# Optimization experiments

Hardware: AMD Instinct MI355X
Metric: run time of the kernel (lower is better)

## Reference

```python
import jax, jax.numpy as jnp
import numpy as np

B, T, NU, NX, NY = 16, 4096, 64, 256, 32

def setup_inputs() -> dict:
    key = jax.random.key(0)
    ks = jax.random.split(key, 7)
    s = 1.0 / np.sqrt(NX)
    return {
        "inputs": jax.random.normal(ks[0], (B, T, NU), dtype=jnp.float32),
        "h0": jax.random.uniform(ks[1], (B, NX), dtype=jnp.float32),
        "H_w": jax.random.normal(ks[2], (NX, NX), dtype=jnp.float32) * s,
        "H_b": jax.random.normal(ks[3], (NX,), dtype=jnp.float32) * s,
        "K_w": jax.random.normal(ks[4], (NX, NU), dtype=jnp.float32) * (1.0 / np.sqrt(NU)),
        "E_inv": jnp.eye(NX, dtype=jnp.float32),  # E = I in the original module
        "out_w": jax.random.normal(ks[5], (NY, NX), dtype=jnp.float32) * s,
        "out_b": jax.random.normal(ks[6], (NY,), dtype=jnp.float32) * s,
    }

def reference(inputs, h0, H_w, H_b, K_w, E_inv, out_w, out_b):
    # Precompute input projections for all steps: [B, T, NX]
    Ku = jnp.einsum("btu,xu->btx", inputs, K_w)
    seq_len = inputs.shape[1]

    def step(ht, ku_t):
        xt = ht @ H_w.T + H_b + ku_t          # Linear(H) + Linear(K)
        ht_new = jax.nn.relu(xt) @ E_inv      # nonlinearity then fixed matrix
        return ht_new, ht_new

    # loop runs seq_len - 1 times; states start with h0
    _, hs = jax.lax.scan(step, h0, jnp.swapaxes(Ku[:, : seq_len - 1, :], 0, 1))
    states = jnp.concatenate([h0[:, None, :], jnp.swapaxes(hs, 0, 1)], axis=1)  # [B, T, NX]
    yest = states @ out_w.T + out_b  # [B, T, NY]
    return (yest, states)
```

## Files before the change

kernel.cpp:

```cpp
#include <hip/hip_runtime.h>

#define Bsz 16
#define Tl  4096
#define NUc 64
#define NXc 256
#define NYc 32

template <int CTRL>
__device__ __forceinline__ float dpp_add(float x) {
    int y = __builtin_amdgcn_update_dpp(0, __float_as_int(x), CTRL, 0xf, 0xf, true);
    return x + __int_as_float(y);
}
__device__ __forceinline__ float reduce8(float x) {
    x = dpp_add<0xB1>(x);
    x = dpp_add<0x4E>(x);
    x = dpp_add<0x141>(x);
    return x;
}
__device__ __forceinline__ float row_reduce16(float x) {
    x = dpp_add<0x128>(x);
    x = dpp_add<0x124>(x);
    x = dpp_add<0x4E>(x);
    x = dpp_add<0xB1>(x);
    return x;
}

__device__ __forceinline__ void fast_barrier() {
    asm volatile("s_waitcnt lgkmcnt(0)\n\ts_barrier" ::: "memory");
}

#define KEEPF(x) asm volatile("" : "+v"(x))

#define DECLW(T,P) \
    float W##T##P##_0,W##T##P##_1,W##T##P##_2,W##T##P##_3,W##T##P##_4,W##T##P##_5,W##T##P##_6,W##T##P##_7, \
          W##T##P##_8,W##T##P##_9,W##T##P##_10,W##T##P##_11,W##T##P##_12,W##T##P##_13,W##T##P##_14,W##T##P##_15
#define LOADW(T,P,RP) { \
    const float* wr_ = (RP) + 16*P; \
    float4 a_=*(const float4*)(wr_+0), b_=*(const float4*)(wr_+4); \
    float4 c_=*(const float4*)(wr_+8), d_=*(const float4*)(wr_+12); \
    W##T##P##_0 =a_.x; W##T##P##_1 =a_.y; W##T##P##_2 =a_.z; W##T##P##_3 =a_.w; \
    W##T##P##_4 =b_.x; W##T##P##_5 =b_.y; W##T##P##_6 =b_.z; W##T##P##_7 =b_.w; \
    W##T##P##_8 =c_.x; W##T##P##_9 =c_.y; W##T##P##_10=c_.z; W##T##P##_11=c_.w; \
    W##T##P##_12=d_.x; W##T##P##_13=d_.y; W##T##P##_14=d_.z; W##T##P##_15=d_.w; }
#define PINW(T,P) \
    KEEPF(W##T##P##_0);  KEEPF(W##T##P##_1);  KEEPF(W##T##P##_2);  KEEPF(W##T##P##_3);  \
    KEEPF(W##T##P##_4);  KEEPF(W##T##P##_5);  KEEPF(W##T##P##_6);  KEEPF(W##T##P##_7);  \
    KEEPF(W##T##P##_8);  KEEPF(W##T##P##_9);  KEEPF(W##T##P##_10); KEEPF(W##T##P##_11); \
    KEEPF(W##T##P##_12); KEEPF(W##T##P##_13); KEEPF(W##T##P##_14); KEEPF(W##T##P##_15)

#define FMAQn(T,P,IA,IB,IC,ID,Q) \
    a##T##0 = fmaf(W##T##P##_##IA, (Q).x, a##T##0); \
    a##T##1 = fmaf(W##T##P##_##IB, (Q).y, a##T##1); \
    a##T##0 = fmaf(W##T##P##_##IC, (Q).z, a##T##0); \
    a##T##1 = fmaf(W##T##P##_##ID, (Q).w, a##T##1)
#define ROWFMA(T) \
    FMAQn(T,0, 0, 1, 2, 3, Q0); FMAQn(T,0, 4, 5, 6, 7, Q1); \
    FMAQn(T,0, 8, 9,10,11, Q2); FMAQn(T,0,12,13,14,15, Q3); \
    FMAQn(T,1, 0, 1, 2, 3, Q4); FMAQn(T,1, 4, 5, 6, 7, Q5); \
    FMAQn(T,1, 8, 9,10,11, Q6); FMAQn(T,1,12,13,14,15, Q7)

#define DECLK8(T) float kk##T##_0,kk##T##_1,kk##T##_2,kk##T##_3,kk##T##_4,kk##T##_5,kk##T##_6,kk##T##_7
#define LOADK8(T,RP) { \
    float4 a_=*(const float4*)(RP), b_=*(const float4*)((RP)+4); \
    kk##T##_0=a_.x; kk##T##_1=a_.y; kk##T##_2=a_.z; kk##T##_3=a_.w; \
    kk##T##_4=b_.x; kk##T##_5=b_.y; kk##T##_6=b_.z; kk##T##_7=b_.w; }
#define PINK8(T) \
    KEEPF(kk##T##_0); KEEPF(kk##T##_1); KEEPF(kk##T##_2); KEEPF(kk##T##_3); \
    KEEPF(kk##T##_4); KEEPF(kk##T##_5); KEEPF(kk##T##_6); KEEPF(kk##T##_7)
#define FMAK8(T) \
    a##T##0=fmaf(kk##T##_0,uu0.x,a##T##0); a##T##1=fmaf(kk##T##_1,uu0.y,a##T##1); \
    a##T##0=fmaf(kk##T##_2,uu0.z,a##T##0); a##T##1=fmaf(kk##T##_3,uu0.w,a##T##1); \
    a##T##0=fmaf(kk##T##_4,uu1.x,a##T##0); a##T##1=fmaf(kk##T##_5,uu1.y,a##T##1); \
    a##T##0=fmaf(kk##T##_6,uu1.z,a##T##0); a##T##1=fmaf(kk##T##_7,uu1.w,a##T##1)

#define KDECL4(Q)  float k##Q##_0, k##Q##_1, k##Q##_2, k##Q##_3
#define KLOAD4(Q) { float4 v_ = *(const float4*)(wr_ + 4*Q); \
    k##Q##_0 = v_.x; k##Q##_1 = v_.y; k##Q##_2 = v_.z; k##Q##_3 = v_.w; }
#define KPIN4(Q)   KEEPF(k##Q##_0); KEEPF(k##Q##_1); KEEPF(k##Q##_2); KEEPF(k##Q##_3)
#define KACC4(Q, U) { \
    s0_ = fmaf(k##Q##_0, (U).x, s0_); s1_ = fmaf(k##Q##_1, (U).y, s1_); \
    s0_ = fmaf(k##Q##_2, (U).z, s0_); s1_ = fmaf(k##Q##_3, (U).w, s1_); }

__global__ __launch_bounds__(256) void ku_kernel(const float* __restrict__ inputs,
                                                 const float* __restrict__ Kw,
                                                 float* __restrict__ Ku) {
    const int x    = threadIdx.x;
    const int row0 = blockIdx.x * 64;

    const float* wr_ = Kw + (size_t)x * NUc;
    KDECL4(0);  KDECL4(1);  KDECL4(2);  KDECL4(3);
    KDECL4(4);  KDECL4(5);  KDECL4(6);  KDECL4(7);
    KDECL4(8);  KDECL4(9);  KDECL4(10); KDECL4(11);
    KDECL4(12); KDECL4(13); KDECL4(14); KDECL4(15);
    KLOAD4(0);  KLOAD4(1);  KLOAD4(2);  KLOAD4(3);
    KLOAD4(4);  KLOAD4(5);  KLOAD4(6);  KLOAD4(7);
    KLOAD4(8);  KLOAD4(9);  KLOAD4(10); KLOAD4(11);
    KLOAD4(12); KLOAD4(13); KLOAD4(14); KLOAD4(15);
    KPIN4(0);  KPIN4(1);  KPIN4(2);  KPIN4(3);
    KPIN4(4);  KPIN4(5);  KPIN4(6);  KPIN4(7);
    KPIN4(8);  KPIN4(9);  KPIN4(10); KPIN4(11);
    KPIN4(12); KPIN4(13); KPIN4(14); KPIN4(15);

    __shared__ float sin_[64 * NUc];
    {
        const float* src = inputs + (size_t)row0 * NUc;
        #pragma unroll
        for (int i = 0; i < 16; ++i)
            sin_[threadIdx.x + i * 256] = src[threadIdx.x + i * 256];
    }
    __syncthreads();

    for (int r = 0; r < 64; ++r) {
        const float4* hp = (const float4*)(&sin_[r * NUc]);
        float s0_ = 0.f, s1_ = 0.f;
        KACC4(0,  hp[0]);  KACC4(1,  hp[1]);  KACC4(2,  hp[2]);  KACC4(3,  hp[3]);
        KACC4(4,  hp[4]);  KACC4(5,  hp[5]);  KACC4(6,  hp[6]);  KACC4(7,  hp[7]);
        KACC4(8,  hp[8]);  KACC4(9,  hp[9]);  KACC4(10, hp[10]); KACC4(11, hp[11]);
        KACC4(12, hp[12]); KACC4(13, hp[13]); KACC4(14, hp[14]); KACC4(15, hp[15]);
        Ku[(size_t)(row0 + r) * NXc + x] = s0_ + s1_;
    }
}

template <bool USE_KU>
__global__ __attribute__((amdgpu_flat_work_group_size(512, 512),
                          amdgpu_waves_per_eu(2, 2)))
void scan6(const float* __restrict__ Ku,
           const float* __restrict__ inputs,
           const float* __restrict__ Kw,
           const float* __restrict__ h0,
           const float* __restrict__ Hw,
           const float* __restrict__ Hb,
           float* __restrict__ states) {
    const int b   = blockIdx.x;
    const int tid = threadIdx.x;
    const int c   = tid & 7;
    const int jg  = tid >> 3;
    const int r0  = 4 * jg;
    const int row_w = r0 + (c & 3);

    __shared__ __align__(16) char shmem[4096];
    char* shm = shmem;
    float* shf = (float*)shmem;

    DECLW(A,0); DECLW(A,1); DECLW(B,0); DECLW(B,1);
    DECLW(C,0); DECLW(C,1); DECLW(D,0); DECLW(D,1);
    {
        const float* p = Hw + (size_t)r0 * NXc + 32 * c;
        LOADW(A,0,p); LOADW(A,1,p);  p += NXc;
        LOADW(B,0,p); LOADW(B,1,p);  p += NXc;
        LOADW(C,0,p); LOADW(C,1,p);  p += NXc;
        LOADW(D,0,p); LOADW(D,1,p);
    }
    DECLK8(A); DECLK8(B); DECLK8(C); DECLK8(D);
    const float* uptr = inputs + (size_t)b * Tl * NUc + 8 * c;
    if (!USE_KU) {
        const float* q = Kw + (size_t)r0 * NUc + 8 * c;
        LOADK8(A,q); q += NUc; LOADK8(B,q); q += NUc;
        LOADK8(C,q); q += NUc; LOADK8(D,q);
    }

    const float bias = Hb[row_w];

    const int wbyte  = 4 * (row_w + 4 * (row_w >> 5));
    const int rbase  = 144 * c;

    const float* kup = Ku + (size_t)b * Tl * NXc + NXc + row_w;
    float*       stp = states + (size_t)b * Tl * NXc + NXc + row_w;

    float bk;
    {
        float h = h0[b * NXc + row_w];
        states[(size_t)b * Tl * NXc + row_w] = h;
        shf[wbyte >> 2] = h;
        bk = USE_KU ? (bias + Ku[(size_t)b * Tl * NXc + row_w]) : bias;
        __syncthreads();
    }

#define STEPBODY(RD, WR) { \
    PINW(A,0); PINW(A,1); PINW(B,0); PINW(B,1); \
    PINW(C,0); PINW(C,1); PINW(D,0); PINW(D,1); \
    if (!USE_KU) { PINK8(A); PINK8(B); PINK8(C); PINK8(D); } \
    const char* rb = shm + (rbase + (RD)); \
    float4 Q0 = *(const float4*)(rb +   0); \
    float4 Q1 = *(const float4*)(rb +  16); \
    float4 Q2 = *(const float4*)(rb +  32); \
    float4 Q3 = *(const float4*)(rb +  48); \
    float4 Q4 = *(const float4*)(rb +  64); \
    float4 Q5 = *(const float4*)(rb +  80); \
    float4 Q6 = *(const float4*)(rb +  96); \
    float4 Q7 = *(const float4*)(rb + 112); \
    float kn_ = 0.f; float4 uu0, uu1; \
    if (USE_KU) { kn_ = *kup; kup += NXc; } \
    else { uu0 = *(const float4*)uptr; uu1 = *(const float4*)(uptr + 4); uptr += NUc; } \
    float aA0=0.f,aA1=0.f,aB0=0.f,aB1=0.f,aC0=0.f,aC1=0.f,aD0=0.f,aD1=0.f; \
    if (!USE_KU) { FMAK8(A); FMAK8(B); FMAK8(C); FMAK8(D); } \
    ROWFMA(A); ROWFMA(B); \
    float rA = reduce8(aA0 + aA1); \
    float rB = reduce8(aB0 + aB1); \
    ROWFMA(C); ROWFMA(D); \
    float rC = reduce8(aC0 + aC1); \
    float rD = reduce8(aD0 + aD1); \
    float x_ = (c & 1) ? rB : rA; \
    float y_ = (c & 1) ? rD : rC; \
    float v_ = (c & 2) ? y_ : x_; \
    float s_ = v_ + bk; \
    float h_ = s_ > 0.f ? s_ : 0.f; \
    *stp = h_; stp += NXc; \
    *(float*)(shm + (wbyte + (WR))) = h_; \
    bk = USE_KU ? (bias + kn_) : bias; \
    fast_barrier(); \
}

    for (int tt = 0; tt < (Tl - 2) / 2; ++tt) {
        STEPBODY(0, 2048);
        STEPBODY(2048, 0);
    }
    STEPBODY(0, 2048);
#undef STEPBODY
}

__global__ __launch_bounds__(512, 2) void yest2(const float* __restrict__ states,
                                                const float* __restrict__ ow,
                                                const float* __restrict__ obv,
                                                float* __restrict__ yest) {
    const int tid = threadIdx.x;
    const int c   = tid & 15;
    const int g   = tid >> 4;

    float y0_,y1_,y2_,y3_,y4_,y5_,y6_,y7_,y8_,y9_,y10_,y11_,y12_,y13_,y14_,y15_;
    {
        const float* wr = ow + (size_t)g * NXc + 16 * c;
        float4 vA = *(const float4*)(wr + 0),  vB = *(const float4*)(wr + 4);
        float4 vC = *(const float4*)(wr + 8),  vD = *(const float4*)(wr + 12);
        y0_=vA.x; y1_=vA.y; y2_ =vA.z; y3_ =vA.w;
        y4_=vB.x; y5_=vB.y; y6_ =vB.z; y7_ =vB.w;
        y8_=vC.x; y9_=vC.y; y10_=vC.z; y11_=vC.w;
        y12_=vD.x;y13_=vD.y;y14_=vD.z; y15_=vD.w;
        KEEPF(y0_); KEEPF(y1_); KEEPF(y2_);  KEEPF(y3_);
        KEEPF(y4_); KEEPF(y5_); KEEPF(y6_);  KEEPF(y7_);
        KEEPF(y8_); KEEPF(y9_); KEEPF(y10_); KEEPF(y11_);
        KEEPF(y12_);KEEPF(y13_);KEEPF(y14_); KEEPF(y15_);
    }
    const float ob = obv[g];

    const int row0 = blockIdx.x * 128;
    for (int r = 0; r < 128; r += 2) {
        const float* s0p = states + (size_t)(row0 + r) * NXc + 16 * c;
        const float* s1p = s0p + NXc;
        float4 A0 = *(const float4*)(s0p + 0), A1 = *(const float4*)(s0p + 4);
        float4 A2 = *(const float4*)(s0p + 8), A3 = *(const float4*)(s0p + 12);
        float4 B0 = *(const float4*)(s1p + 0), B1 = *(const float4*)(s1p + 4);
        float4 B2 = *(const float4*)(s1p + 8), B3 = *(const float4*)(s1p + 12);
        float acc0 = y0_*A0.x + y1_*A0.y + y2_*A0.z + y3_*A0.w
                   + y4_*A1.x + y5_*A1.y + y6_*A1.z + y7_*A1.w
                   + y8_*A2.x + y9_*A2.y + y10_*A2.z + y11_*A2.w
                   + y12_*A3.x + y13_*A3.y + y14_*A3.z + y15_*A3.w;
        float acc1 = y0_*B0.x + y1_*B0.y + y2_*B0.z + y3_*B0.w
                   + y4_*B1.x + y5_*B1.y + y6_*B1.z + y7_*B1.w
                   + y8_*B2.x + y9_*B2.y + y10_*B2.z + y11_*B2.w
                   + y12_*B3.x + y13_*B3.y + y14_*B3.z + y15_*B3.w;
        acc0 = row_reduce16(acc0);
        acc1 = row_reduce16(acc1);
        if (c == 0) {
            yest[(size_t)(row0 + r)     * NYc + g] = acc0 + ob;
            yest[(size_t)(row0 + r + 1) * NYc + g] = acc1 + ob;
        }
    }
}

extern "C" void kernel_launch(void* const* d_in, const int* in_sizes, int n_in,
                              void* d_out, int out_size, void* d_ws, size_t ws_size,
                              hipStream_t stream) {
    const float* inputs = (const float*)d_in[0];
    const float* h0     = (const float*)d_in[1];
    const float* Hw     = (const float*)d_in[2];
    const float* Hb     = (const float*)d_in[3];
    const float* Kw     = (const float*)d_in[4];
    const float* ow     = (const float*)d_in[6];
    const float* ob     = (const float*)d_in[7];

    float* yest   = (float*)d_out;
    float* states = (float*)d_out + (size_t)Bsz * Tl * NYc;

    const size_t ku_bytes = (size_t)Bsz * Tl * NXc * sizeof(float);
    const int    nrows    = Bsz * Tl;

    if (ws_size >= ku_bytes) {
        float* Ku = (float*)d_ws;
        ku_kernel<<<dim3(nrows / 64), dim3(256), 0, stream>>>(inputs, Kw, Ku);
        scan6<true><<<dim3(Bsz), dim3(512), 0, stream>>>(Ku, inputs, Kw, h0, Hw, Hb, states);
    } else {
        scan6<false><<<dim3(Bsz), dim3(512), 0, stream>>>(nullptr, inputs, Kw, h0, Hw, Hb, states);
    }
    yest2<<<dim3(nrows / 128), dim3(512), 0, stream>>>(states, ow, ob, yest);
}
```

Measured before the change: 1.985 ms.

## Interleave scan column chunks, prefetch first chunk across barrier, batch DPP reductions

```diff
diff --git a/kernel.cpp b/kernel.cpp
--- a/kernel.cpp
+++ b/kernel.cpp
@@ -10,12 +10,6 @@
 __device__ __forceinline__ float dpp_add(float x) {
     int y = __builtin_amdgcn_update_dpp(0, __float_as_int(x), CTRL, 0xf, 0xf, true);
     return x + __int_as_float(y);
-}
-__device__ __forceinline__ float reduce8(float x) {
-    x = dpp_add<0xB1>(x);
-    x = dpp_add<0x4E>(x);
-    x = dpp_add<0x141>(x);
-    return x;
 }
 __device__ __forceinline__ float row_reduce16(float x) {
     x = dpp_add<0x128>(x);
@@ -25,39 +19,46 @@
     return x;
 }
 
-__device__ __forceinline__ void fast_barrier() {
-    asm volatile("s_waitcnt lgkmcnt(0)\n\ts_barrier" ::: "memory");
+__device__ __forceinline__ void red8x4(float sA, float sB, float sC, float sD,
+                                       float& rA, float& rB, float& rC, float& rD) {
+    asm("v_add_f32_dpp %0, %4, %4 quad_perm:[1,0,3,2] row_mask:0xf bank_mask:0xf\n\t"
+        "v_add_f32_dpp %1, %5, %5 quad_perm:[1,0,3,2] row_mask:0xf bank_mask:0xf\n\t"
+        "v_add_f32_dpp %2, %6, %6 quad_perm:[1,0,3,2] row_mask:0xf bank_mask:0xf\n\t"
+        "v_add_f32_dpp %3, %7, %7 quad_perm:[1,0,3,2] row_mask:0xf bank_mask:0xf\n\t"
+        "v_add_f32_dpp %0, %0, %0 quad_perm:[2,3,0,1] row_mask:0xf bank_mask:0xf\n\t"
+        "v_add_f32_dpp %1, %1, %1 quad_perm:[2,3,0,1] row_mask:0xf bank_mask:0xf\n\t"
+        "v_add_f32_dpp %2, %2, %2 quad_perm:[2,3,0,1] row_mask:0xf bank_mask:0xf\n\t"
+        "v_add_f32_dpp %3, %3, %3 quad_perm:[2,3,0,1] row_mask:0xf bank_mask:0xf\n\t"
+        "v_add_f32_dpp %0, %0, %0 row_half_mirror row_mask:0xf bank_mask:0xf\n\t"
+        "v_add_f32_dpp %1, %1, %1 row_half_mirror row_mask:0xf bank_mask:0xf\n\t"
+        "v_add_f32_dpp %2, %2, %2 row_half_mirror row_mask:0xf bank_mask:0xf\n\t"
+        "v_add_f32_dpp %3, %3, %3 row_half_mirror row_mask:0xf bank_mask:0xf"
+        : "=&v"(rA), "=&v"(rB), "=&v"(rC), "=&v"(rD)
+        : "v"(sA), "v"(sB), "v"(sC), "v"(sD));
 }
 
 #define KEEPF(x) asm volatile("" : "+v"(x))
 
-#define DECLW(T,P) \
-    float W##T##P##_0,W##T##P##_1,W##T##P##_2,W##T##P##_3,W##T##P##_4,W##T##P##_5,W##T##P##_6,W##T##P##_7, \
-          W##T##P##_8,W##T##P##_9,W##T##P##_10,W##T##P##_11,W##T##P##_12,W##T##P##_13,W##T##P##_14,W##T##P##_15
-#define LOADW(T,P,RP) { \
-    const float* wr_ = (RP) + 16*P; \
-    float4 a_=*(const float4*)(wr_+0), b_=*(const float4*)(wr_+4); \
-    float4 c_=*(const float4*)(wr_+8), d_=*(const float4*)(wr_+12); \
-    W##T##P##_0 =a_.x; W##T##P##_1 =a_.y; W##T##P##_2 =a_.z; W##T##P##_3 =a_.w; \
-    W##T##P##_4 =b_.x; W##T##P##_5 =b_.y; W##T##P##_6 =b_.z; W##T##P##_7 =b_.w; \
-    W##T##P##_8 =c_.x; W##T##P##_9 =c_.y; W##T##P##_10=c_.z; W##T##P##_11=c_.w; \
-    W##T##P##_12=d_.x; W##T##P##_13=d_.y; W##T##P##_14=d_.z; W##T##P##_15=d_.w; }
-#define PINW(T,P) \
-    KEEPF(W##T##P##_0);  KEEPF(W##T##P##_1);  KEEPF(W##T##P##_2);  KEEPF(W##T##P##_3);  \
-    KEEPF(W##T##P##_4);  KEEPF(W##T##P##_5);  KEEPF(W##T##P##_6);  KEEPF(W##T##P##_7);  \
-    KEEPF(W##T##P##_8);  KEEPF(W##T##P##_9);  KEEPF(W##T##P##_10); KEEPF(W##T##P##_11); \
-    KEEPF(W##T##P##_12); KEEPF(W##T##P##_13); KEEPF(W##T##P##_14); KEEPF(W##T##P##_15)
-
-#define FMAQn(T,P,IA,IB,IC,ID,Q) \
-    a##T##0 = fmaf(W##T##P##_##IA, (Q).x, a##T##0); \
-    a##T##1 = fmaf(W##T##P##_##IB, (Q).y, a##T##1); \
-    a##T##0 = fmaf(W##T##P##_##IC, (Q).z, a##T##0); \
-    a##T##1 = fmaf(W##T##P##_##ID, (Q).w, a##T##1)
-#define ROWFMA(T) \
-    FMAQn(T,0, 0, 1, 2, 3, Q0); FMAQn(T,0, 4, 5, 6, 7, Q1); \
-    FMAQn(T,0, 8, 9,10,11, Q2); FMAQn(T,0,12,13,14,15, Q3); \
-    FMAQn(T,1, 0, 1, 2, 3, Q4); FMAQn(T,1, 4, 5, 6, 7, Q5); \
-    FMAQn(T,1, 8, 9,10,11, Q6); FMAQn(T,1,12,13,14,15, Q7)
+#define DECLC(T,J) float W##T##J##_0, W##T##J##_1, W##T##J##_2, W##T##J##_3
+#define LOADC(T,J,P) { float4 v_ = *(const float4*)(P); \
+    W##T##J##_0=v_.x; W##T##J##_1=v_.y; W##T##J##_2=v_.z; W##T##J##_3=v_.w; }
+#define PINC(T,J) KEEPF(W##T##J##_0); KEEPF(W##T##J##_1); \
+                  KEEPF(W##T##J##_2); KEEPF(W##T##J##_3)
+#define FMAC4(T,J,Q) \
+    a##T##0 = fmaf(W##T##J##_0, (Q).x, a##T##0); \
+    a##T##1 = fmaf(W##T##J##_1, (Q).y, a##T##1); \
+    a##T##0 = fmaf(W##T##J##_2, (Q).z, a##T##0); \
+    a##T##1 = fmaf(W##T##J##_3, (Q).w, a##T##1)
+
+#define DECL8(T) DECLC(T,0); DECLC(T,1); DECLC(T,2); DECLC(T,3); \
+                 DECLC(T,4); DECLC(T,5); DECLC(T,6); DECLC(T,7)
+#define LOAD8(T,RP) \
+    LOADC(T,0,(RP)+4*q0); LOADC(T,1,(RP)+4*q1); LOADC(T,2,(RP)+4*q2); \
+    LOADC(T,3,(RP)+4*q3); LOADC(T,4,(RP)+4*q4); LOADC(T,5,(RP)+4*q5); \
+    LOADC(T,6,(RP)+4*q6); LOADC(T,7,(RP)+4*q7)
+#define PIN8(T) PINC(T,0); PINC(T,1); PINC(T,2); PINC(T,3); \
+                PINC(T,4); PINC(T,5); PINC(T,6); PINC(T,7)
+#define CHUNKF(J,Q) FMAC4(A,J,Q); FMAC4(B,J,Q); FMAC4(C,J,Q); FMAC4(D,J,Q)
 
 #define DECLK8(T) float kk##T##_0,kk##T##_1,kk##T##_2,kk##T##_3,kk##T##_4,kk##T##_5,kk##T##_6,kk##T##_7
 #define LOADK8(T,RP) { \
@@ -124,7 +125,7 @@
 template <bool USE_KU>
 __global__ __attribute__((amdgpu_flat_work_group_size(512, 512),
                           amdgpu_waves_per_eu(2, 2)))
-void scan6(const float* __restrict__ Ku,
+void scan7(const float* __restrict__ Ku,
            const float* __restrict__ inputs,
            const float* __restrict__ Kw,
            const float* __restrict__ h0,
@@ -135,21 +136,34 @@
     const int tid = threadIdx.x;
     const int c   = tid & 7;
     const int jg  = tid >> 3;
+    const int w   = tid >> 6;
     const int r0  = 4 * jg;
     const int row_w = r0 + (c & 3);
 
-    __shared__ __align__(16) char shmem[4096];
+    __shared__ __align__(16) char shmem[4608];
     char* shm = shmem;
-    float* shf = (float*)shmem;
-
-    DECLW(A,0); DECLW(A,1); DECLW(B,0); DECLW(B,1);
-    DECLW(C,0); DECLW(C,1); DECLW(D,0); DECLW(D,1);
+
+    const int p0   = 8 * w + c;
+    const int q0 = p0,               q1 = (p0 +  8) & 63;
+    const int q2 = (p0 + 16) & 63,   q3 = (p0 + 24) & 63;
+    const int q4 = (p0 + 32) & 63,   q5 = (p0 + 40) & 63;
+    const int q6 = (p0 + 48) & 63,   q7 = (p0 + 56) & 63;
+    const int rdv   = 16 * (p0 + (p0 >> 3));
+    const int wslot = row_w + 4 * (row_w >> 5);
+    const int wrv   = 4 * wslot + ((c & 4) ? 1152 : 0);
+
+    const char* rb0 = shm + rdv;
+    const char* rb1 = shm + rdv + 2304;
+    char*       wb0 = shm + wrv;
+    char*       wb1 = shm + wrv + 2304;
+
+    DECL8(A); DECL8(B); DECL8(C); DECL8(D);
     {
-        const float* p = Hw + (size_t)r0 * NXc + 32 * c;
-        LOADW(A,0,p); LOADW(A,1,p);  p += NXc;
-        LOADW(B,0,p); LOADW(B,1,p);  p += NXc;
-        LOADW(C,0,p); LOADW(C,1,p);  p += NXc;
-        LOADW(D,0,p); LOADW(D,1,p);
+        const float* pA = Hw + (size_t)(r0 + 0) * NXc;
+        const float* pB = Hw + (size_t)(r0 + 1) * NXc;
+        const float* pC = Hw + (size_t)(r0 + 2) * NXc;
+        const float* pD = Hw + (size_t)(r0 + 3) * NXc;
+        LOAD8(A, pA); LOAD8(B, pB); LOAD8(C, pC); LOAD8(D, pD);
     }
     DECLK8(A); DECLK8(B); DECLK8(C); DECLK8(D);
     const float* uptr = inputs + (size_t)b * Tl * NUc + 8 * c;
@@ -160,62 +174,59 @@
     }
 
     const float bias = Hb[row_w];
-
-    const int wbyte  = 4 * (row_w + 4 * (row_w >> 5));
-    const int rbase  = 144 * c;
-
     const float* kup = Ku + (size_t)b * Tl * NXc + NXc + row_w;
     float*       stp = states + (size_t)b * Tl * NXc + NXc + row_w;
 
     float bk;
+    float4 Q0c;
     {
         float h = h0[b * NXc + row_w];
         states[(size_t)b * Tl * NXc + row_w] = h;
-        shf[wbyte >> 2] = h;
+        *(float*)wb0 = h;
+        Q0c = *(const float4*)rb0;
         bk = USE_KU ? (bias + Ku[(size_t)b * Tl * NXc + row_w]) : bias;
         __syncthreads();
     }
 
-#define STEPBODY(RD, WR) { \
-    PINW(A,0); PINW(A,1); PINW(B,0); PINW(B,1); \
-    PINW(C,0); PINW(C,1); PINW(D,0); PINW(D,1); \
+#define STEPBODY(RB, WB, RBN) { \
+    PIN8(A); PIN8(B); PIN8(C); PIN8(D); \
     if (!USE_KU) { PINK8(A); PINK8(B); PINK8(C); PINK8(D); } \
-    const char* rb = shm + (rbase + (RD)); \
-    float4 Q0 = *(const float4*)(rb +   0); \
-    float4 Q1 = *(const float4*)(rb +  16); \
-    float4 Q2 = *(const float4*)(rb +  32); \
-    float4 Q3 = *(const float4*)(rb +  48); \
-    float4 Q4 = *(const float4*)(rb +  64); \
-    float4 Q5 = *(const float4*)(rb +  80); \
-    float4 Q6 = *(const float4*)(rb +  96); \
-    float4 Q7 = *(const float4*)(rb + 112); \
+    float4 Q1 = *(const float4*)((RB) + 144); \
+    float4 Q2 = *(const float4*)((RB) + 288); \
+    float4 Q3 = *(const float4*)((RB) + 432); \
+    float4 Q4 = *(const float4*)((RB) + 576); \
+    float4 Q5 = *(const float4*)((RB) + 720); \
+    float4 Q6 = *(const float4*)((RB) + 864); \
+    float4 Q7 = *(const float4*)((RB) + 1008); \
     float kn_ = 0.f; float4 uu0, uu1; \
     if (USE_KU) { kn_ = *kup; kup += NXc; } \
     else { uu0 = *(const float4*)uptr; uu1 = *(const float4*)(uptr + 4); uptr += NUc; } \
     float aA0=0.f,aA1=0.f,aB0=0.f,aB1=0.f,aC0=0.f,aC1=0.f,aD0=0.f,aD1=0.f; \
+    CHUNKF(0, Q0c); \
     if (!USE_KU) { FMAK8(A); FMAK8(B); FMAK8(C); FMAK8(D); } \
-    ROWFMA(A); ROWFMA(B); \
-    float rA = reduce8(aA0 + aA1); \
-    float rB = reduce8(aB0 + aB1); \
-    ROWFMA(C); ROWFMA(D); \
-    float rC = reduce8(aC0 + aC1); \
-    float rD = reduce8(aD0 + aD1); \
+    CHUNKF(1, Q1); CHUNKF(2, Q2); CHUNKF(3, Q3); CHUNKF(4, Q4); \
+    CHUNKF(5, Q5); CHUNKF(6, Q6); CHUNKF(7, Q7); \
+    float sA = aA0 + aA1, sB = aB0 + aB1; \
+    float sC = aC0 + aC1, sD = aD0 + aD1; \
+    float rA, rB, rC, rD; \
+    red8x4(sA, sB, sC, sD, rA, rB, rC, rD); \
     float x_ = (c & 1) ? rB : rA; \
     float y_ = (c & 1) ? rD : rC; \
     float v_ = (c & 2) ? y_ : x_; \
     float s_ = v_ + bk; \
     float h_ = s_ > 0.f ? s_ : 0.f; \
-    *stp = h_; stp += NXc; \
-    *(float*)(shm + (wbyte + (WR))) = h_; \
+    *(float*)(WB) = h_;                     \
+    Q0c = *(const float4*)(RBN);            \
+    *stp = h_; stp += NXc;                  \
     bk = USE_KU ? (bias + kn_) : bias; \
-    fast_barrier(); \
+    asm volatile("s_waitcnt lgkmcnt(1)\n\ts_barrier" ::: "memory"); \
 }
 
     for (int tt = 0; tt < (Tl - 2) / 2; ++tt) {
-        STEPBODY(0, 2048);
-        STEPBODY(2048, 0);
-    }
-    STEPBODY(0, 2048);
+        STEPBODY(rb0, wb1, rb1);
+        STEPBODY(rb1, wb0, rb0);
+    }
+    STEPBODY(rb0, wb1, rb1);
 #undef STEPBODY
 }
 
@@ -288,9 +299,9 @@
     if (ws_size >= ku_bytes) {
         float* Ku = (float*)d_ws;
         ku_kernel<<<dim3(nrows / 64), dim3(256), 0, stream>>>(inputs, Kw, Ku);
-        scan6<true><<<dim3(Bsz), dim3(512), 0, stream>>>(Ku, inputs, Kw, h0, Hw, Hb, states);
+        scan7<true><<<dim3(Bsz), dim3(512), 0, stream>>>(Ku, inputs, Kw, h0, Hw, Hb, states);
     } else {
-        scan6<false><<<dim3(Bsz), dim3(512), 0, stream>>>(nullptr, inputs, Kw, h0, Hw, Hb, states);
+        scan7<false><<<dim3(Bsz), dim3(512), 0, stream>>>(nullptr, inputs, Kw, h0, Hw, Hb, states);
     }
     yest2<<<dim3(nrows / 128), dim3(512), 0, stream>>>(states, ow, ob, yest);
 }
```

Result: no change. 1.947 ms (-1.9%).
